# Kernel tuning notes

Hardware: AMD Instinct MI355X
Metric: run time of the kernel (lower is better)

Reference implementation:

```python
import jax, jax.numpy as jnp
import numpy as np

C = 1.0  # Poincare ball curvature
EPS = 1e-15


def setup_inputs() -> dict:
    key = jax.random.key(0)
    k1, k2, k3 = jax.random.split(key, 3)
    B, S, D_IN, D_OUT = 16, 8192, 128, 128
    # points strictly inside the unit ball: ||x|| ~ 0.05*sqrt(128) ~ 0.57
    x = 0.05 * jax.random.normal(k1, (B, S, D_IN), dtype=jnp.float32)
    z = 0.01 * jax.random.normal(k2, (D_IN, D_OUT), dtype=jnp.float32)  # init_std=0.01 normal
    r = 0.01 * jax.random.normal(k3, (D_OUT,), dtype=jnp.float32)
    return {"x": x, "z": z, "r": r}


def reference(x, z, r):
    # Poincare MLR (Shimizu et al., Hyperbolic NN++), as in hypll PoincareBall.mlr
    c = jnp.asarray(C, x.dtype)
    cs = jnp.sqrt(c)
    prefix = x.shape[:-1]
    x2 = x.reshape(-1, x.shape[-1])                       # [N, d_in]
    # conformal factor lambda_x = 2 / (1 - c ||x||^2)
    lam = 2.0 / (1.0 - c * jnp.sum(x2 * x2, axis=-1, keepdims=True))  # [N, 1]
    z_norm = jnp.maximum(jnp.linalg.norm(z, axis=0), EPS)             # [d_out]
    two_csr = 2.0 * cs * r                                            # [d_out]
    inner = x2 @ z                                                    # [N, d_out]
    arg = (cs * lam * inner / z_norm) * jnp.cosh(two_csr) - (lam - 1.0) * jnp.sinh(two_csr)
    out = (2.0 * z_norm / cs) * jnp.arcsinh(arg)                      # [N, d_out]
    return out.reshape(*prefix, z.shape[1])
```

## Files before the change

kernel.cpp:

```cpp
#include <hip/hip_runtime.h>
#include <cstdint>


typedef __attribute__((ext_vector_type(8))) short short8;
typedef __attribute__((ext_vector_type(4))) float floatx4;

#define D 128
#define ZT_STRIDE 136

__device__ inline unsigned bf16_rne(float f) {
    unsigned u = __float_as_uint(f);
    return ((u + 0x7FFFu + ((u >> 16) & 1u)) >> 16) & 0xFFFFu;
}

__global__ void hmlr_prep(const float* __restrict__ z, const float* __restrict__ r,
                          unsigned short* __restrict__ zt, float* __restrict__ An,
                          float* __restrict__ Bn, float* __restrict__ Sn) {
    int n = blockIdx.x;
    int k = threadIdx.x;
    float v = z[k * D + n];
    zt[n * ZT_STRIDE + k] = (unsigned short)bf16_rne(v);
    float p = v * v;
    #pragma unroll
    for (int off = 32; off >= 1; off >>= 1) p += __shfl_down(p, off, 64);
    __shared__ float tmp[2];
    if ((k & 63) == 0) tmp[k >> 6] = p;
    __syncthreads();
    if (k == 0) {
        float ss = tmp[0] + tmp[1];
        float zn = fmaxf(sqrtf(ss), 1e-15f);
        float tc = 2.0f * r[n];
        An[n] = coshf(tc) / zn;
        Bn[n] = sinhf(tc);
        Sn[n] = 2.0f * zn;
    }
}

__global__ __launch_bounds__(256) void hmlr_main(const float* __restrict__ x,
                                                 const unsigned short* __restrict__ zt,
                                                 const float* __restrict__ An,
                                                 const float* __restrict__ Bn,
                                                 const float* __restrict__ Sn,
                                                 float* __restrict__ out) {
    const int t    = threadIdx.x;
    const int w    = t >> 6;
    const int l    = t & 63;
    const int quad = l >> 4;
    const int l15  = l & 15;

    const int rowbase = blockIdx.x * 64 + w * 16;
    const int myrow   = rowbase + l15;

    const float* xrow = x + (size_t)myrow * D + quad * 8;
    float4 xv[8];
    #pragma unroll
    for (int kc = 0; kc < 4; ++kc) {
        xv[2 * kc]     = *reinterpret_cast<const float4*>(xrow + kc * 32);
        xv[2 * kc + 1] = *reinterpret_cast<const float4*>(xrow + kc * 32 + 4);
    }

    float ssq = 0.f;
    #pragma unroll
    for (int i = 0; i < 8; ++i)
        ssq += xv[i].x * xv[i].x + xv[i].y * xv[i].y + xv[i].z * xv[i].z + xv[i].w * xv[i].w;
    ssq += __shfl_xor(ssq, 16);
    ssq += __shfl_xor(ssq, 32);

    short8 afrag[4];
    #pragma unroll
    for (int kc = 0; kc < 4; ++kc) {
        float4 v0 = xv[2 * kc], v1 = xv[2 * kc + 1];
        union { short8 s8; unsigned short u[8]; } af;
        af.u[0] = (unsigned short)bf16_rne(v0.x);
        af.u[1] = (unsigned short)bf16_rne(v0.y);
        af.u[2] = (unsigned short)bf16_rne(v0.z);
        af.u[3] = (unsigned short)bf16_rne(v0.w);
        af.u[4] = (unsigned short)bf16_rne(v1.x);
        af.u[5] = (unsigned short)bf16_rne(v1.y);
        af.u[6] = (unsigned short)bf16_rne(v1.z);
        af.u[7] = (unsigned short)bf16_rne(v1.w);
        afrag[kc] = af.s8;
    }

    floatx4 acc[8];
    #pragma unroll
    for (int nt = 0; nt < 8; ++nt) acc[nt] = (floatx4){0.f, 0.f, 0.f, 0.f};

    #pragma unroll
    for (int kc = 0; kc < 4; ++kc) {
        const unsigned short* zb = zt + kc * 32 + quad * 8;
        #pragma unroll
        for (int nt = 0; nt < 8; ++nt) {
            short8 b = *reinterpret_cast<const short8*>(zb + (nt * 16 + l15) * ZT_STRIDE);
            acc[nt] = __builtin_amdgcn_mfma_f32_16x16x32_bf16(afrag[kc], b, acc[nt], 0, 0, 0);
        }
    }

    float anv[8], bnv[8], snv[8];
    #pragma unroll
    for (int nt = 0; nt < 8; ++nt) {
        int n = nt * 16 + l15;
        anv[nt] = An[n];
        bnv[nt] = Bn[n];
        snv[nt] = Sn[n];
    }
    #pragma unroll
    for (int reg = 0; reg < 4; ++reg) {
        float rss = __shfl(ssq, quad * 4 + reg);
        float lam = 2.0f / (1.0f - rss);
        float lm1 = lam - 1.0f;
        float* orow = out + (size_t)(rowbase + quad * 4 + reg) * D + l15;
        #pragma unroll
        for (int nt = 0; nt < 8; ++nt) {
            float inner = acc[nt][reg];
            float arg = __fmaf_rn(lam * inner, anv[nt], -lm1 * bnv[nt]);
            float a   = fabsf(arg);
            float as  = __logf(a + __fsqrt_rn(__fmaf_rn(a, a, 1.0f)));
            orow[nt * 16] = copysignf(as, arg) * snv[nt];
        }
    }
}

extern "C" void kernel_launch(void* const* d_in, const int* in_sizes, int n_in,
                              void* d_out, int out_size, void* d_ws, size_t ws_size,
                              hipStream_t stream) {
    const float* x = (const float*)d_in[0];
    const float* z = (const float*)d_in[1];
    const float* r = (const float*)d_in[2];
    float* out = (float*)d_out;

    char* wsb = (char*)d_ws;
    unsigned short* zt = (unsigned short*)wsb;
    float* An = (float*)(wsb + 128 * ZT_STRIDE * sizeof(unsigned short));
    float* Bn = An + 128;
    float* Sn = An + 256;

    hmlr_prep<<<128, 128, 0, stream>>>(z, r, zt, An, Bn, Sn);

    const int n_rows = in_sizes[0] / D;
    hmlr_main<<<n_rows / 64, 256, 0, stream>>>(x, zt, An, Bn, Sn, out);
}
```

Before: 140.3 us.

## Stage x and z tiles through swizzled LDS with coalesced loads and larger blocks

The main kernel now loads x with fully coalesced float4 reads and writes it as bf16 into a swizzled LDS tile, from which the MFMA A fragments are read. The whole bf16 z matrix goes into swizzled LDS once per block, replacing the strided global B-fragment reads. Blocks grow to 512 threads covering 128 rows, and the three per-column constants are packed into one float4. This is meant to cut uncoalesced global traffic, at the cost of 64KB of LDS per block, which limits occupancy, plus extra shuffles to recover row norms.

```diff
diff --git a/kernel.cpp b/kernel.cpp
--- a/kernel.cpp
+++ b/kernel.cpp
@@ -6,7 +6,6 @@
 typedef __attribute__((ext_vector_type(4))) float floatx4;
 
 #define D 128
-#define ZT_STRIDE 136
 
 __device__ inline unsigned bf16_rne(float f) {
     unsigned u = __float_as_uint(f);
@@ -14,12 +13,11 @@
 }
 
 __global__ void hmlr_prep(const float* __restrict__ z, const float* __restrict__ r,
-                          unsigned short* __restrict__ zt, float* __restrict__ An,
-                          float* __restrict__ Bn, float* __restrict__ Sn) {
+                          unsigned short* __restrict__ zt, float4* __restrict__ abs4) {
     int n = blockIdx.x;
     int k = threadIdx.x;
     float v = z[k * D + n];
-    zt[n * ZT_STRIDE + k] = (unsigned short)bf16_rne(v);
+    zt[n * D + k] = (unsigned short)bf16_rne(v);
     float p = v * v;
     #pragma unroll
     for (int off = 32; off >= 1; off >>= 1) p += __shfl_down(p, off, 64);
@@ -30,57 +28,86 @@
         float ss = tmp[0] + tmp[1];
         float zn = fmaxf(sqrtf(ss), 1e-15f);
         float tc = 2.0f * r[n];
-        An[n] = coshf(tc) / zn;
-        Bn[n] = sinhf(tc);
-        Sn[n] = 2.0f * zn;
+        abs4[n] = make_float4(coshf(tc) / zn, sinhf(tc), 2.0f * zn, 0.0f);
     }
 }
 
-__global__ __launch_bounds__(256) void hmlr_main(const float* __restrict__ x,
-                                                 const unsigned short* __restrict__ zt,
-                                                 const float* __restrict__ An,
-                                                 const float* __restrict__ Bn,
-                                                 const float* __restrict__ Sn,
-                                                 float* __restrict__ out) {
+__global__ __launch_bounds__(512, 4) void hmlr_main(const float* __restrict__ x,
+                                                    const unsigned short* __restrict__ zt,
+                                                    const float4* __restrict__ abs4,
+                                                    float* __restrict__ out) {
+    __shared__ __align__(16) unsigned char lds[65536];
+    #define LDS_Z 32768
+
     const int t    = threadIdx.x;
     const int w    = t >> 6;
     const int l    = t & 63;
     const int quad = l >> 4;
     const int l15  = l & 15;
+    const int l7   = l15 & 7;
 
-    const int rowbase = blockIdx.x * 64 + w * 16;
-    const int myrow   = rowbase + l15;
+    const int rowbase = blockIdx.x * 128 + w * 16;
 
-    const float* xrow = x + (size_t)myrow * D + quad * 8;
+    const uint4* ztg = reinterpret_cast<const uint4*>(zt);
+    uint4 zreg[4];
+    #pragma unroll
+    for (int i = 0; i < 4; ++i) zreg[i] = ztg[t + (i << 9)];
+
+    const float4* xg = reinterpret_cast<const float4*>(x) + (size_t)blockIdx.x * 4096 + w * 512;
     float4 xv[8];
     #pragma unroll
-    for (int kc = 0; kc < 4; ++kc) {
-        xv[2 * kc]     = *reinterpret_cast<const float4*>(xrow + kc * 32);
-        xv[2 * kc + 1] = *reinterpret_cast<const float4*>(xrow + kc * 32 + 4);
+    for (int j = 0; j < 8; ++j) xv[j] = xg[(j << 6) + l];
+
+    float s[8];
+    #pragma unroll
+    for (int j = 0; j < 8; ++j) {
+        float4 v = xv[j];
+        int f   = (j << 6) + l;
+        int row = w * 16 + (f >> 5);
+        int fc  = f & 31;
+        float p = v.x * v.x + v.y * v.y + v.z * v.z + v.w * v.w;
+        p += __shfl_xor(p, 1);
+        p += __shfl_xor(p, 2);
+        p += __shfl_xor(p, 4);
+        p += __shfl_xor(p, 8);
+        p += __shfl_xor(p, 16);
+        s[j] = p;
+        unsigned lo = bf16_rne(v.x) | (bf16_rne(v.y) << 16);
+        unsigned hi = bf16_rne(v.z) | (bf16_rne(v.w) << 16);
+        int byte = (row << 8) + ((((fc >> 1) ^ (row & 7)) << 4)) + ((fc & 1) << 3);
+        *reinterpret_cast<uint2*>(&lds[byte]) = make_uint2(lo, hi);
     }
 
-    float ssq = 0.f;
-    #pragma unroll
-    for (int i = 0; i < 8; ++i)
-        ssq += xv[i].x * xv[i].x + xv[i].y * xv[i].y + xv[i].z * xv[i].z + xv[i].w * xv[i].w;
-    ssq += __shfl_xor(ssq, 16);
-    ssq += __shfl_xor(ssq, 32);
+    int idx3 = (l >> 1) & 7;
+    float a0 = (idx3 & 1) ? s[1] : s[0];
+    float a1 = (idx3 & 1) ? s[3] : s[2];
+    float a2 = (idx3 & 1) ? s[5] : s[4];
+    float a3 = (idx3 & 1) ? s[7] : s[6];
+    float b0 = (idx3 & 2) ? a1 : a0;
+    float b1 = (idx3 & 2) ? a3 : a2;
+    float vsel = (idx3 & 4) ? b1 : b0;
+    float usel = __shfl_xor(vsel, 32);
+    float rq = (((l >> 5) & 1) == (l & 1)) ? vsel : usel;
 
     short8 afrag[4];
     #pragma unroll
     for (int kc = 0; kc < 4; ++kc) {
-        float4 v0 = xv[2 * kc], v1 = xv[2 * kc + 1];
-        union { short8 s8; unsigned short u[8]; } af;
-        af.u[0] = (unsigned short)bf16_rne(v0.x);
-        af.u[1] = (unsigned short)bf16_rne(v0.y);
-        af.u[2] = (unsigned short)bf16_rne(v0.z);
-        af.u[3] = (unsigned short)bf16_rne(v0.w);
-        af.u[4] = (unsigned short)bf16_rne(v1.x);
-        af.u[5] = (unsigned short)bf16_rne(v1.y);
-        af.u[6] = (unsigned short)bf16_rne(v1.z);
-        af.u[7] = (unsigned short)bf16_rne(v1.w);
-        afrag[kc] = af.s8;
+        int byte = ((w * 16 + l15) << 8) + (((quad + (kc << 2)) ^ l7) << 4);
+        afrag[kc] = *reinterpret_cast<const short8*>(&lds[byte]);
     }
+
+    #pragma unroll
+    for (int i = 0; i < 4; ++i) {
+        int idx = t + (i << 9);
+        int row = idx >> 4, c = idx & 15;
+        int byte = LDS_Z + (row << 8) + (((c ^ (row & 7)) << 4));
+        *reinterpret_cast<uint4*>(&lds[byte]) = zreg[i];
+    }
+    __syncthreads();
+
+    float4 cst[8];
+    #pragma unroll
+    for (int nt = 0; nt < 8; ++nt) cst[nt] = abs4[nt * 16 + l15];
 
     floatx4 acc[8];
     #pragma unroll
@@ -88,37 +115,30 @@
 
     #pragma unroll
     for (int kc = 0; kc < 4; ++kc) {
-        const unsigned short* zb = zt + kc * 32 + quad * 8;
         #pragma unroll
         for (int nt = 0; nt < 8; ++nt) {
-            short8 b = *reinterpret_cast<const short8*>(zb + (nt * 16 + l15) * ZT_STRIDE);
+            int byte = LDS_Z + ((nt * 16 + l15) << 8) + (((quad + (kc << 2)) ^ l7) << 4);
+            short8 b = *reinterpret_cast<const short8*>(&lds[byte]);
             acc[nt] = __builtin_amdgcn_mfma_f32_16x16x32_bf16(afrag[kc], b, acc[nt], 0, 0, 0);
         }
     }
 
-    float anv[8], bnv[8], snv[8];
-    #pragma unroll
-    for (int nt = 0; nt < 8; ++nt) {
-        int n = nt * 16 + l15;
-        anv[nt] = An[n];
-        bnv[nt] = Bn[n];
-        snv[nt] = Sn[n];
-    }
     #pragma unroll
     for (int reg = 0; reg < 4; ++reg) {
-        float rss = __shfl(ssq, quad * 4 + reg);
+        float rss = __shfl(rq, (quad << 2) | reg);
         float lam = 2.0f / (1.0f - rss);
         float lm1 = lam - 1.0f;
-        float* orow = out + (size_t)(rowbase + quad * 4 + reg) * D + l15;
+        float* orow = out + (size_t)(rowbase + (quad << 2) + reg) * D + l15;
         #pragma unroll
         for (int nt = 0; nt < 8; ++nt) {
             float inner = acc[nt][reg];
-            float arg = __fmaf_rn(lam * inner, anv[nt], -lm1 * bnv[nt]);
+            float arg = __fmaf_rn(lam * inner, cst[nt].x, -lm1 * cst[nt].y);
             float a   = fabsf(arg);
             float as  = __logf(a + __fsqrt_rn(__fmaf_rn(a, a, 1.0f)));
-            orow[nt * 16] = copysignf(as, arg) * snv[nt];
+            orow[nt * 16] = copysignf(as, arg) * cst[nt].z;
         }
     }
+    #undef LDS_Z
 }
 
 extern "C" void kernel_launch(void* const* d_in, const int* in_sizes, int n_in,
@@ -131,12 +151,10 @@
 
     char* wsb = (char*)d_ws;
     unsigned short* zt = (unsigned short*)wsb;
-    float* An = (float*)(wsb + 128 * ZT_STRIDE * sizeof(unsigned short));
-    float* Bn = An + 128;
-    float* Sn = An + 256;
+    float4* abs4 = (float4*)(wsb + 128 * D * sizeof(unsigned short));
 
-    hmlr_prep<<<128, 128, 0, stream>>>(z, r, zt, An, Bn, Sn);
+    hmlr_prep<<<128, 128, 0, stream>>>(z, r, zt, abs4);
 
     const int n_rows = in_sizes[0] / D;
-    hmlr_main<<<n_rows / 64, 256, 0, stream>>>(x, zt, An, Bn, Sn, out);
+    hmlr_main<<<n_rows / 128, 512, 0, stream>>>(x, zt, abs4, out);
 }
```

Result: faster. 125.4 us (-10.6%).

## Stage swizzled bf16 weights in LDS and pack per-column constants

Applied to the files above, without the earlier changes.

Weights are now written in an XOR-swizzled layout and each block copies the whole 32 KB bf16 weight matrix into LDS with global_load_lds. B fragments are then read from LDS without bank conflicts instead of from global/L2. The per-column constants are packed into one float4 with ln2 folded in so log2 can replace log. The bf16 conversion now rounds half-up with simpler bit ops, and launch bounds ask for 5 blocks per CU. The trade-off is a 32 KB LDS fill per block, which adds latency and can limit occupancy, plus slightly different rounding.

```diff
diff --git a/kernel.cpp b/kernel.cpp
--- a/kernel.cpp
+++ b/kernel.cpp
@@ -6,57 +6,74 @@
 typedef __attribute__((ext_vector_type(4))) float floatx4;
 
 #define D 128
-#define ZT_STRIDE 136
 
-__device__ inline unsigned bf16_rne(float f) {
-    unsigned u = __float_as_uint(f);
-    return ((u + 0x7FFFu + ((u >> 16) & 1u)) >> 16) & 0xFFFFu;
+__device__ inline unsigned bf16_rhu(float f) {
+    return (__float_as_uint(f) + 0x8000u) >> 16;
+}
+__device__ inline unsigned pack2(float lo, float hi) {
+    return bf16_rhu(lo) | (bf16_rhu(hi) << 16);
 }
 
 __global__ void hmlr_prep(const float* __restrict__ z, const float* __restrict__ r,
-                          unsigned short* __restrict__ zt, float* __restrict__ An,
-                          float* __restrict__ Bn, float* __restrict__ Sn) {
+                          unsigned short* __restrict__ zt_sw, float4* __restrict__ abs4) {
     int n = blockIdx.x;
     int k = threadIdx.x;
     float v = z[k * D + n];
-    zt[n * ZT_STRIDE + k] = (unsigned short)bf16_rne(v);
-    float p = v * v;
+    int c = k >> 3, p = k & 7;
+    zt_sw[n * D + ((c ^ (n & 7)) << 3) + p] = (unsigned short)bf16_rhu(v);
+    float pw = v * v;
     #pragma unroll
-    for (int off = 32; off >= 1; off >>= 1) p += __shfl_down(p, off, 64);
+    for (int off = 32; off >= 1; off >>= 1) pw += __shfl_down(pw, off, 64);
     __shared__ float tmp[2];
-    if ((k & 63) == 0) tmp[k >> 6] = p;
+    if ((k & 63) == 0) tmp[k >> 6] = pw;
     __syncthreads();
     if (k == 0) {
         float ss = tmp[0] + tmp[1];
         float zn = fmaxf(sqrtf(ss), 1e-15f);
         float tc = 2.0f * r[n];
-        An[n] = coshf(tc) / zn;
-        Bn[n] = sinhf(tc);
-        Sn[n] = 2.0f * zn;
+        abs4[n] = make_float4(coshf(tc) / zn, sinhf(tc),
+                              2.0f * zn * 0.69314718055994531f, 0.0f);
     }
 }
 
-__global__ __launch_bounds__(256) void hmlr_main(const float* __restrict__ x,
-                                                 const unsigned short* __restrict__ zt,
-                                                 const float* __restrict__ An,
-                                                 const float* __restrict__ Bn,
-                                                 const float* __restrict__ Sn,
-                                                 float* __restrict__ out) {
+__global__ __launch_bounds__(256, 5) void hmlr_main(const float* __restrict__ x,
+                                                    const unsigned short* __restrict__ zt_sw,
+                                                    const float4* __restrict__ abs4,
+                                                    float* __restrict__ out) {
+    __shared__ __align__(16) unsigned char lds[32768];
+
     const int t    = threadIdx.x;
     const int w    = t >> 6;
     const int l    = t & 63;
     const int quad = l >> 4;
     const int l15  = l & 15;
+    const int l7   = l & 7;
+
+#if __has_builtin(__builtin_amdgcn_global_load_lds)
+    #pragma unroll
+    for (int i = 0; i < 8; ++i) {
+        int ci = w * 512 + i * 64 + l;
+        __builtin_amdgcn_global_load_lds(
+            (const __attribute__((address_space(1))) unsigned int*)(zt_sw + (ci << 3)),
+            (__attribute__((address_space(3))) unsigned int*)(lds + ((w * 512 + i * 64) << 4)),
+            16, 0, 0);
+    }
+#else
+    #pragma unroll
+    for (int i = 0; i < 8; ++i) {
+        int ci = w * 512 + i * 64 + l;
+        *reinterpret_cast<uint4*>(&lds[ci << 4]) = reinterpret_cast<const uint4*>(zt_sw)[ci];
+    }
+#endif
+    __syncthreads();
 
     const int rowbase = blockIdx.x * 64 + w * 16;
-    const int myrow   = rowbase + l15;
-
-    const float* xrow = x + (size_t)myrow * D + quad * 8;
+    const float* xrow = x + (size_t)(rowbase + l15) * D + (quad << 3);
     float4 xv[8];
     #pragma unroll
     for (int kc = 0; kc < 4; ++kc) {
-        xv[2 * kc]     = *reinterpret_cast<const float4*>(xrow + kc * 32);
-        xv[2 * kc + 1] = *reinterpret_cast<const float4*>(xrow + kc * 32 + 4);
+        xv[2 * kc]     = *reinterpret_cast<const float4*>(xrow + (kc << 5));
+        xv[2 * kc + 1] = *reinterpret_cast<const float4*>(xrow + (kc << 5) + 4);
     }
 
     float ssq = 0.f;
@@ -69,16 +86,11 @@
     short8 afrag[4];
     #pragma unroll
     for (int kc = 0; kc < 4; ++kc) {
-        float4 v0 = xv[2 * kc], v1 = xv[2 * kc + 1];
-        union { short8 s8; unsigned short u[8]; } af;
-        af.u[0] = (unsigned short)bf16_rne(v0.x);
-        af.u[1] = (unsigned short)bf16_rne(v0.y);
-        af.u[2] = (unsigned short)bf16_rne(v0.z);
-        af.u[3] = (unsigned short)bf16_rne(v0.w);
-        af.u[4] = (unsigned short)bf16_rne(v1.x);
-        af.u[5] = (unsigned short)bf16_rne(v1.y);
-        af.u[6] = (unsigned short)bf16_rne(v1.z);
-        af.u[7] = (unsigned short)bf16_rne(v1.w);
+        union { short8 s8; unsigned u[4]; } af;
+        af.u[0] = pack2(xv[2 * kc].x,     xv[2 * kc].y);
+        af.u[1] = pack2(xv[2 * kc].z,     xv[2 * kc].w);
+        af.u[2] = pack2(xv[2 * kc + 1].x, xv[2 * kc + 1].y);
+        af.u[3] = pack2(xv[2 * kc + 1].z, xv[2 * kc + 1].w);
         afrag[kc] = af.s8;
     }
 
@@ -88,35 +100,32 @@
 
     #pragma unroll
     for (int kc = 0; kc < 4; ++kc) {
-        const unsigned short* zb = zt + kc * 32 + quad * 8;
+        short8 b[8];
+        #pragma unroll
+        for (int nt = 0; nt < 8; ++nt)
+            b[nt] = *reinterpret_cast<const short8*>(
+                &lds[((nt * 16 + l15) << 8) + (((quad + (kc << 2)) ^ l7) << 4)]);
+        #pragma unroll
+        for (int nt = 0; nt < 8; ++nt)
+            acc[nt] = __builtin_amdgcn_mfma_f32_16x16x32_bf16(afrag[kc], b[nt], acc[nt], 0, 0, 0);
+    }
+
+    float4 cst[8];
+    #pragma unroll
+    for (int nt = 0; nt < 8; ++nt) cst[nt] = abs4[nt * 16 + l15];
+
+    #pragma unroll
+    for (int reg = 0; reg < 4; ++reg) {
+        float rss = __shfl(ssq, (quad << 2) | reg);
+        float lam = 2.0f / (1.0f - rss);
+        float lm1 = lam - 1.0f;
+        float* orow = out + (size_t)(rowbase + (quad << 2) + reg) * D + l15;
         #pragma unroll
         for (int nt = 0; nt < 8; ++nt) {
-            short8 b = *reinterpret_cast<const short8*>(zb + (nt * 16 + l15) * ZT_STRIDE);
-            acc[nt] = __builtin_amdgcn_mfma_f32_16x16x32_bf16(afrag[kc], b, acc[nt], 0, 0, 0);
-        }
-    }
-
-    float anv[8], bnv[8], snv[8];
-    #pragma unroll
-    for (int nt = 0; nt < 8; ++nt) {
-        int n = nt * 16 + l15;
-        anv[nt] = An[n];
-        bnv[nt] = Bn[n];
-        snv[nt] = Sn[n];
-    }
-    #pragma unroll
-    for (int reg = 0; reg < 4; ++reg) {
-        float rss = __shfl(ssq, quad * 4 + reg);
-        float lam = 2.0f / (1.0f - rss);
-        float lm1 = lam - 1.0f;
-        float* orow = out + (size_t)(rowbase + quad * 4 + reg) * D + l15;
-        #pragma unroll
-        for (int nt = 0; nt < 8; ++nt) {
-            float inner = acc[nt][reg];
-            float arg = __fmaf_rn(lam * inner, anv[nt], -lm1 * bnv[nt]);
+            float arg = __fmaf_rn(lam * acc[nt][reg], cst[nt].x, -lm1 * cst[nt].y);
             float a   = fabsf(arg);
-            float as  = __logf(a + __fsqrt_rn(__fmaf_rn(a, a, 1.0f)));
-            orow[nt * 16] = copysignf(as, arg) * snv[nt];
+            float as  = __log2f(a + __fsqrt_rn(__fmaf_rn(a, a, 1.0f)));
+            orow[nt * 16] = copysignf(as, arg) * cst[nt].z;
         }
     }
 }
@@ -130,13 +139,11 @@
     float* out = (float*)d_out;
 
     char* wsb = (char*)d_ws;
-    unsigned short* zt = (unsigned short*)wsb;
-    float* An = (float*)(wsb + 128 * ZT_STRIDE * sizeof(unsigned short));
-    float* Bn = An + 128;
-    float* Sn = An + 256;
+    unsigned short* zt_sw = (unsigned short*)wsb;
+    float4* abs4 = (float4*)(wsb + 128 * D * sizeof(unsigned short));
 
-    hmlr_prep<<<128, 128, 0, stream>>>(z, r, zt, An, Bn, Sn);
+    hmlr_prep<<<128, 128, 0, stream>>>(z, r, zt_sw, abs4);
 
     const int n_rows = in_sizes[0] / D;
-    hmlr_main<<<n_rows / 64, 256, 0, stream>>>(x, zt, An, Bn, Sn, out);
+    hmlr_main<<<n_rows / 64, 256, 0, stream>>>(x, zt_sw, abs4, out);
 }
```

New measurement: 121.0 us. 13.7% less time.
